# Kernel tuning notes

Measured on AMD Instinct MI355X. Metric: run time of the kernel, lower is better.

Reference implementation:

```python
import jax, jax.numpy as jnp
import numpy as np

B, L, H, P = 16, 4096, 512, 256
LN_EPS = 1e-6  # flax nnx.LayerNorm default


def setup_inputs() -> dict:
    key = jax.random.key(0)
    ks = jax.random.split(key, 9)
    dt_min, dt_max = 1e-3, 1e-1
    x = jax.random.normal(ks[0], (B, L, H), dtype=jnp.float32)
    # lecun-normal-like scaling for B (fan_in = H) and C (fan_in = P)
    return {
        "x": x,
        "log_lambda_re": jax.random.normal(ks[1], (P,), dtype=jnp.float32),
        "lambda_im": jax.random.normal(ks[2], (P,), dtype=jnp.float32) * 3.0,
        "B_re": jax.random.normal(ks[3], (P, H), dtype=jnp.float32) / np.sqrt(H),
        "B_im": jax.random.normal(ks[4], (P, H), dtype=jnp.float32) / np.sqrt(H),
        "C_re": jax.random.normal(ks[5], (H, P), dtype=jnp.float32) / np.sqrt(P),
        "C_im": jax.random.normal(ks[6], (H, P), dtype=jnp.float32) / np.sqrt(P),
        "D": jax.random.normal(ks[7], (H,), dtype=jnp.float32),
        "log_step": jax.random.uniform(ks[8], (P,), dtype=jnp.float32)
        * (np.log(dt_max) - np.log(dt_min)) + np.log(dt_min),
        "ln_scale": jnp.ones((H,), dtype=jnp.float32),
        "ln_bias": jnp.zeros((H,), dtype=jnp.float32),
    }


def _binary_operator(q_i, q_j):
    A_i, b_i = q_i
    A_j, b_j = q_j
    return (A_j * A_i, A_j * b_i + b_j)


def reference(x, log_lambda_re, lambda_im, B_re, B_im, C_re, C_im, D, log_step,
              ln_scale, ln_bias):
    Lambda = -jnp.exp(log_lambda_re) + 1j * lambda_im          # [P] complex
    B_tilde = B_re + 1j * B_im                                  # [P,H]
    C_tilde = C_re + 1j * C_im                                  # [H,P]
    step = jnp.exp(log_step)                                    # [P]
    # ZOH discretization
    Lambda_bar = jnp.exp(Lambda * step)                         # [P]
    B_bar = ((Lambda_bar - 1.0) / Lambda)[:, None] * B_tilde    # [P,H]
    # SSM via parallel associative scan over the length axis
    Bu = x @ B_bar.T                                            # [B,L,P] complex
    Lambda_el = jnp.broadcast_to(Lambda_bar, Bu.shape)          # [B,L,P]
    _, xs = jax.lax.associative_scan(_binary_operator, (Lambda_el, Bu), axis=-2)
    ys = 2.0 * (xs @ C_tilde.T).real                            # [B,L,H]
    y = ys + x * D
    y = jax.nn.gelu(y)
    # residual + LayerNorm
    z = x + y
    mean = jnp.mean(z, axis=-1, keepdims=True)
    var = jnp.var(z, axis=-1, keepdims=True)
    return (z - mean) * jax.lax.rsqrt(var + LN_EPS) * ln_scale + ln_bias
```

## Files before the change

### kernel.cpp

```cpp
#include <hip/hip_runtime.h>
#include <hip/hip_bf16.h>
#include <cstdint>
#include <cstddef>

typedef short bf16x8 __attribute__((ext_vector_type(8)));
typedef float f32x4  __attribute__((ext_vector_type(4)));

#define HH 512
#define PP 256
#define LL 4096
#define BBATCH 16
#define MM (BBATCH * LL)
#define NCHUNK 128
#define SCHUNK 32

__device__ __forceinline__ unsigned short f2bf(float f) {
  union { float f; unsigned u; } v; v.f = f;
  unsigned r = (v.u + 0x7FFFu + ((v.u >> 16) & 1u)) >> 16;
  return (unsigned short)r;
}
__device__ __forceinline__ float bf2f(unsigned short b) {
  return __uint_as_float(((unsigned)b) << 16);
}

__device__ __forceinline__ void async16(const void* g, void* l) {
  __builtin_amdgcn_global_load_lds(
      (const __attribute__((address_space(1))) unsigned*)g,
      (__attribute__((address_space(3))) unsigned*)l, 16, 0, 0);
}

__global__ void precompute_params(const float* __restrict__ llr_,
                                  const float* __restrict__ lim_,
                                  const float* __restrict__ lstep_,
                                  float* __restrict__ lam) {
  int p = threadIdx.x;
  if (p >= PP) return;
  float Lr = -expf(llr_[p]);
  float Li = lim_[p];
  float st = expf(lstep_[p]);
  float mag = expf(Lr * st);
  float ang = Li * st;
  float lbr = mag * cosf(ang);
  float lbi = mag * sinf(ang);
  float den = Lr * Lr + Li * Li;
  float nr = lbr - 1.f, ni = lbi;
  float cr = (nr * Lr + ni * Li) / den;
  float ci = (ni * Lr - nr * Li) / den;
  float m32 = expf(32.f * Lr * st);
  float a32r = m32 * cosf(32.f * ang);
  float a32i = m32 * sinf(32.f * ang);
  lam[p]            = lbr;
  lam[PP + p]       = lbi;
  lam[2 * PP + p]   = a32r;
  lam[3 * PP + p]   = a32i;
  lam[4 * PP + p]   = cr;
  lam[5 * PP + p]   = ci;
}

__global__ void build_weights(const float* __restrict__ B_re,
                              const float* __restrict__ B_im,
                              const float* __restrict__ C_re,
                              const float* __restrict__ C_im,
                              const float* __restrict__ lam,
                              unsigned short* __restrict__ Bcat,
                              unsigned short* __restrict__ Ccat) {
  int bid = blockIdx.x;
  int tid = threadIdx.x;
  if (bid < 512) {
    int n = bid;
    int p = (n < PP) ? n : n - PP;
    float cr = lam[4 * PP + p], ci = lam[5 * PP + p];
    for (int c = tid; c < HH; c += 256) {
      float br = B_re[(size_t)p * HH + c];
      float bi = B_im[(size_t)p * HH + c];
      float v = (n < PP) ? (cr * br - ci * bi) : (cr * bi + ci * br);
      Bcat[(size_t)n * HH + c] = f2bf(v);
    }
  } else {
    int h = bid - 512;
    for (int c = tid; c < HH; c += 256) {
      float v = (c < PP) ? 2.f * C_re[(size_t)h * PP + c]
                         : -2.f * C_im[(size_t)h * PP + (c - PP)];
      Ccat[(size_t)h * HH + c] = f2bf(v);
    }
  }
}

__global__ __launch_bounds__(256) void cvt_x_bf16(const float* __restrict__ x,
                                                  unsigned short* __restrict__ xb) {
  const float4* x4 = (const float4*)x;
  ushort4* o4 = (ushort4*)xb;
  int stride = 2048 * 256;
  for (int i = blockIdx.x * 256 + threadIdx.x; i < (MM * HH / 4); i += stride) {
    float4 v = x4[i];
    ushort4 o;
    o.x = f2bf(v.x); o.y = f2bf(v.y); o.z = f2bf(v.z); o.w = f2bf(v.w);
    o4[i] = o;
  }
}

template <int EPI>
__global__ __launch_bounds__(256) void gemm_bt(const unsigned short* __restrict__ A,
                                               const unsigned short* __restrict__ Bt,
                                               const unsigned short* xf,
                                               const float* __restrict__ Dv,
                                               unsigned short* Cout) {
  __shared__ __align__(16) unsigned short Asl[128 * 64];
  __shared__ __align__(16) unsigned short Bsl[128 * 64];
  const int tid = threadIdx.x, lane = tid & 63, w = tid >> 6;
  const int bid = blockIdx.x;
  const int logical = (bid & 7) * 256 + (bid >> 3);
  const int mt = logical >> 2, nt = logical & 3;
  const int m0 = mt * 128, n0 = nt * 128;
  const int r = lane & 15, g = lane >> 4;
  const int wm = (w >> 1) * 64, wn = (w & 1) * 64;

  const char* Ab = (const char*)A;
  const char* Bb = (const char*)Bt;
  char* AslB = (char*)Asl;
  char* BslB = (char*)Bsl;

  f32x4 acc[4][4];
#pragma unroll
  for (int a = 0; a < 4; ++a)
#pragma unroll
    for (int b = 0; b < 4; ++b) acc[a][b] = (f32x4){0.f, 0.f, 0.f, 0.f};

  const int swz = (r & 7) << 4;

  for (int kt = 0; kt < 512; kt += 64) {
#pragma unroll
    for (int j = 0; j < 4; ++j) {
      int idx = w * 4 + j;
      int W = idx * 1024 + lane * 16;
      int row = W >> 7;
      int colb = (W & 127) ^ ((row & 7) << 4);
      async16(Ab + (size_t)(m0 + row) * 1024 + kt * 2 + colb, AslB + W);
      async16(Bb + (size_t)(n0 + row) * 1024 + kt * 2 + colb, BslB + W);
    }
    asm volatile("s_waitcnt vmcnt(0)" ::: "memory");
    __syncthreads();
#pragma unroll
    for (int kk = 0; kk < 2; ++kk) {
      bf16x8 af[4], bv[4];
#pragma unroll
      for (int mi = 0; mi < 4; ++mi)
        af[mi] = *(const bf16x8*)(AslB + (wm + mi * 16 + r) * 128 +
                                  ((kk * 64 + g * 16) ^ swz));
#pragma unroll
      for (int ni = 0; ni < 4; ++ni)
        bv[ni] = *(const bf16x8*)(BslB + (wn + ni * 16 + r) * 128 +
                                  ((kk * 64 + g * 16) ^ swz));
#pragma unroll
      for (int mi = 0; mi < 4; ++mi)
#pragma unroll
        for (int ni = 0; ni < 4; ++ni)
          acc[mi][ni] = __builtin_amdgcn_mfma_f32_16x16x32_bf16(
              af[mi], bv[ni], acc[mi][ni], 0, 0, 0);
    }
    __syncthreads();
  }

#pragma unroll
  for (int mi = 0; mi < 4; ++mi) {
#pragma unroll
    for (int ni = 0; ni < 4; ++ni) {
      int col = n0 + wn + ni * 16 + r;
      float Dh = (EPI == 1) ? Dv[col] : 0.f;
#pragma unroll
      for (int j = 0; j < 4; ++j) {
        int row = m0 + wm + mi * 16 + g * 4 + j;
        float v = acc[mi][ni][j];
        if (EPI == 0) {
          Cout[(size_t)row * 512 + col] = f2bf(v);
        } else {
          float xv = bf2f(xf[(size_t)row * 512 + col]);
          float t = v + xv * Dh;
          float u = 0.7978845608028654f * (t + 0.044715f * t * t * t);
          float e = __expf(2.f * u);
          float th = 1.f - 2.f / (e + 1.f);
          float y = 0.5f * t * (1.f + th);
          Cout[(size_t)row * 512 + col] = f2bf(xv + y);
        }
      }
    }
  }
}

__global__ __launch_bounds__(256) void scan_carry(const unsigned short* __restrict__ Bu,
                                                  const float* __restrict__ lam,
                                                  float* __restrict__ carry) {
  int bid = blockIdx.x;
  int b = bid >> 7, c = bid & 127;
  int p = threadIdx.x;
  float ar = lam[p], ai = lam[PP + p];
  float sr = 0.f, si = 0.f;
  size_t base = ((size_t)b * LL + (size_t)c * SCHUNK) * 512;
#pragma unroll
  for (int i = 0; i < SCHUNK; ++i) {
    float ur = bf2f(Bu[base + (size_t)i * 512 + p]);
    float ui = bf2f(Bu[base + (size_t)i * 512 + 256 + p]);
    float nr = ar * sr - ai * si + ur;
    float ni = ar * si + ai * sr + ui;
    sr = nr; si = ni;
  }
  carry[(size_t)bid * 512 + p] = sr;
  carry[(size_t)bid * 512 + 256 + p] = si;
}

__global__ void scan_chain(float* __restrict__ carry, const float* __restrict__ lam) {
  int b = blockIdx.x;
  int p = threadIdx.x;
  float a32r = lam[2 * PP + p], a32i = lam[3 * PP + p];
  float sr = 0.f, si = 0.f;
  for (int c = 0; c < NCHUNK; ++c) {
    size_t idx = (size_t)(b * NCHUNK + c) * 512;
    float cr = carry[idx + p], ci = carry[idx + 256 + p];
    carry[idx + p] = sr;
    carry[idx + 256 + p] = si;
    float nr = cr + a32r * sr - a32i * si;
    float ni = ci + a32r * si + a32i * sr;
    sr = nr; si = ni;
  }
}

__global__ __launch_bounds__(256) void scan_final(const unsigned short* Bu,
                                                  const float* __restrict__ lam,
                                                  const float* __restrict__ carry,
                                                  unsigned short* xs) {
  int bid = blockIdx.x;
  int b = bid >> 7, c = bid & 127;
  int p = threadIdx.x;
  float ar = lam[p], ai = lam[PP + p];
  size_t cidx = (size_t)bid * 512;
  float sr = carry[cidx + p], si = carry[cidx + 256 + p];
  size_t base = ((size_t)b * LL + (size_t)c * SCHUNK) * 512;
#pragma unroll
  for (int i = 0; i < SCHUNK; ++i) {
    float ur = bf2f(Bu[base + (size_t)i * 512 + p]);
    float ui = bf2f(Bu[base + (size_t)i * 512 + 256 + p]);
    float nr = ar * sr - ai * si + ur;
    float ni = ar * si + ai * sr + ui;
    sr = nr; si = ni;
    xs[base + (size_t)i * 512 + p] = f2bf(sr);
    xs[base + (size_t)i * 512 + 256 + p] = f2bf(si);
  }
}

__global__ __launch_bounds__(256) void ln_kernel(const unsigned short* __restrict__ z,
                                                 const float* __restrict__ scale,
                                                 const float* __restrict__ bias,
                                                 float* __restrict__ out) {
  int tid = threadIdx.x, lane = tid & 63, wv = tid >> 6;
  int gw = blockIdx.x * 4 + wv;
  int c0 = lane * 8;
  float sc[8], bi[8];
#pragma unroll
  for (int j = 0; j < 8; ++j) { sc[j] = scale[c0 + j]; bi[j] = bias[c0 + j]; }
  for (int row = gw; row < MM; row += 8192) {
    uint4 zv = *(const uint4*)(z + (size_t)row * 512 + c0);
    float f[8];
    f[0] = __uint_as_float(zv.x << 16); f[1] = __uint_as_float(zv.x & 0xFFFF0000u);
    f[2] = __uint_as_float(zv.y << 16); f[3] = __uint_as_float(zv.y & 0xFFFF0000u);
    f[4] = __uint_as_float(zv.z << 16); f[5] = __uint_as_float(zv.z & 0xFFFF0000u);
    f[6] = __uint_as_float(zv.w << 16); f[7] = __uint_as_float(zv.w & 0xFFFF0000u);
    float s = 0.f, s2 = 0.f;
#pragma unroll
    for (int j = 0; j < 8; ++j) { s += f[j]; s2 += f[j] * f[j]; }
#pragma unroll
    for (int o = 32; o; o >>= 1) {
      s += __shfl_xor(s, o, 64);
      s2 += __shfl_xor(s2, o, 64);
    }
    float mean = s * (1.f / 512.f);
    float var = s2 * (1.f / 512.f) - mean * mean;
    float inv = rsqrtf(var + 1e-6f);
    float o8[8];
#pragma unroll
    for (int j = 0; j < 8; ++j) o8[j] = (f[j] - mean) * inv * sc[j] + bi[j];
    float4* op = (float4*)(out + (size_t)row * 512 + c0);
    op[0] = make_float4(o8[0], o8[1], o8[2], o8[3]);
    op[1] = make_float4(o8[4], o8[5], o8[6], o8[7]);
  }
}

extern "C" void kernel_launch(void* const* d_in, const int* in_sizes, int n_in,
                              void* d_out, int out_size, void* d_ws, size_t ws_size,
                              hipStream_t stream) {
  const float* x    = (const float*)d_in[0];
  const float* llr  = (const float*)d_in[1];
  const float* lim  = (const float*)d_in[2];
  const float* B_re = (const float*)d_in[3];
  const float* B_im = (const float*)d_in[4];
  const float* C_re = (const float*)d_in[5];
  const float* C_im = (const float*)d_in[6];
  const float* Dv   = (const float*)d_in[7];
  const float* lstep= (const float*)d_in[8];
  const float* lnsc = (const float*)d_in[9];
  const float* lnbi = (const float*)d_in[10];
  float* out = (float*)d_out;

  char* ws = (char*)d_ws;
  unsigned short* xb   = (unsigned short*)(ws);
  unsigned short* bu   = (unsigned short*)(ws + 67108864);
  unsigned short* bcat = (unsigned short*)(ws + 134217728);
  unsigned short* ccat = (unsigned short*)(ws + 134742016);
  float* lam           = (float*)(ws + 135266304);
  float* carry         = (float*)(ws + 135272448);

  precompute_params<<<1, 256, 0, stream>>>(llr, lim, lstep, lam);
  build_weights<<<1024, 256, 0, stream>>>(B_re, B_im, C_re, C_im, lam, bcat, ccat);
  cvt_x_bf16<<<2048, 256, 0, stream>>>(x, xb);
  gemm_bt<0><<<2048, 256, 0, stream>>>(xb, bcat, nullptr, nullptr, bu);
  scan_carry<<<2048, 256, 0, stream>>>(bu, lam, carry);
  scan_chain<<<16, 256, 0, stream>>>(carry, lam);
  scan_final<<<2048, 256, 0, stream>>>(bu, lam, carry, bu);
  gemm_bt<1><<<2048, 256, 0, stream>>>(bu, ccat, xb, Dv, xb);
  ln_kernel<<<2048, 256, 0, stream>>>(xb, lnsc, lnbi, out);
}
```

Baseline: 476.5 us.

## Double-buffer GEMM loads, interleave re/im in Bu, split carry chain hierarchically

The GEMM becomes persistent over four M tiles per block with double-buffered LDS. The next k-stage's async global-to-LDS loads are issued before the current stage's MFMAs, to overlap load latency with compute. Real and imaginary parts of Bu and xs are interleaved so each scan thread does one 32-bit load and store instead of two strided halves, and the weights are reordered to match. The serial 128-step carry chain on 16 blocks is replaced by a three-level scan (group reduce, 16-step chain using Lambda^256, group fixup) to add parallelism. The cost is fewer GEMM blocks (512), more LDS per block and two extra small launches.

```diff
diff --git a/kernel.cpp b/kernel.cpp
--- a/kernel.cpp
+++ b/kernel.cpp
@@ -13,6 +13,8 @@
 #define MM (BBATCH * LL)
 #define NCHUNK 128
 #define SCHUNK 32
+#define NGRP 16
+#define GCH 8
 
 __device__ __forceinline__ unsigned short f2bf(float f) {
   union { float f; unsigned u; } v; v.f = f;
@@ -49,12 +51,17 @@
   float m32 = expf(32.f * Lr * st);
   float a32r = m32 * cosf(32.f * ang);
   float a32i = m32 * sinf(32.f * ang);
+  float m256 = expf(256.f * Lr * st);
+  float a256r = m256 * cosf(256.f * ang);
+  float a256i = m256 * sinf(256.f * ang);
   lam[p]            = lbr;
   lam[PP + p]       = lbi;
   lam[2 * PP + p]   = a32r;
   lam[3 * PP + p]   = a32i;
   lam[4 * PP + p]   = cr;
   lam[5 * PP + p]   = ci;
+  lam[6 * PP + p]   = a256r;
+  lam[7 * PP + p]   = a256i;
 }
 
 __global__ void build_weights(const float* __restrict__ B_re,
@@ -68,19 +75,21 @@
   int tid = threadIdx.x;
   if (bid < 512) {
     int n = bid;
-    int p = (n < PP) ? n : n - PP;
+    int p = n >> 1;
+    int is_re = !(n & 1);
     float cr = lam[4 * PP + p], ci = lam[5 * PP + p];
     for (int c = tid; c < HH; c += 256) {
       float br = B_re[(size_t)p * HH + c];
       float bi = B_im[(size_t)p * HH + c];
-      float v = (n < PP) ? (cr * br - ci * bi) : (cr * bi + ci * br);
+      float v = is_re ? (cr * br - ci * bi) : (cr * bi + ci * br);
       Bcat[(size_t)n * HH + c] = f2bf(v);
     }
   } else {
     int h = bid - 512;
     for (int c = tid; c < HH; c += 256) {
-      float v = (c < PP) ? 2.f * C_re[(size_t)h * PP + c]
-                         : -2.f * C_im[(size_t)h * PP + (c - PP)];
+      int p = c >> 1;
+      float v = !(c & 1) ? 2.f * C_re[(size_t)h * PP + p]
+                         : -2.f * C_im[(size_t)h * PP + p];
       Ccat[(size_t)h * HH + c] = f2bf(v);
     }
   }
@@ -105,51 +114,67 @@
                                                const unsigned short* xf,
                                                const float* __restrict__ Dv,
                                                unsigned short* Cout) {
-  __shared__ __align__(16) unsigned short Asl[128 * 64];
-  __shared__ __align__(16) unsigned short Bsl[128 * 64];
+  __shared__ __align__(16) unsigned short As[2][8192];
+  __shared__ __align__(16) unsigned short Bs[2][8192];
   const int tid = threadIdx.x, lane = tid & 63, w = tid >> 6;
   const int bid = blockIdx.x;
-  const int logical = (bid & 7) * 256 + (bid >> 3);
-  const int mt = logical >> 2, nt = logical & 3;
-  const int m0 = mt * 128, n0 = nt * 128;
+  const int logical = (bid & 7) * 64 + (bid >> 3);
+  const int nt = logical & 3, mg = logical >> 2;
+  const int n0 = nt * 128;
   const int r = lane & 15, g = lane >> 4;
   const int wm = (w >> 1) * 64, wn = (w & 1) * 64;
-
+  const int swz = (r & 7) << 4;
+
+  int sW[4], srow[4], scol[4];
+#pragma unroll
+  for (int j = 0; j < 4; ++j) {
+    int idx = w * 4 + j;
+    int W = idx * 1024 + lane * 16;
+    sW[j] = W;
+    srow[j] = W >> 7;
+    scol[j] = (W & 127) ^ (((W >> 7) & 7) << 4);
+  }
   const char* Ab = (const char*)A;
   const char* Bb = (const char*)Bt;
-  char* AslB = (char*)Asl;
-  char* BslB = (char*)Bsl;
+  char* As0 = (char*)&As[0][0];
+  char* Bs0 = (char*)&Bs[0][0];
 
   f32x4 acc[4][4];
 #pragma unroll
-  for (int a = 0; a < 4; ++a)
-#pragma unroll
-    for (int b = 0; b < 4; ++b) acc[a][b] = (f32x4){0.f, 0.f, 0.f, 0.f};
-
-  const int swz = (r & 7) << 4;
-
-  for (int kt = 0; kt < 512; kt += 64) {
-#pragma unroll
-    for (int j = 0; j < 4; ++j) {
-      int idx = w * 4 + j;
-      int W = idx * 1024 + lane * 16;
-      int row = W >> 7;
-      int colb = (W & 127) ^ ((row & 7) << 4);
-      async16(Ab + (size_t)(m0 + row) * 1024 + kt * 2 + colb, AslB + W);
-      async16(Bb + (size_t)(n0 + row) * 1024 + kt * 2 + colb, BslB + W);
-    }
-    asm volatile("s_waitcnt vmcnt(0)" ::: "memory");
-    __syncthreads();
+  for (int a2 = 0; a2 < 4; ++a2)
+#pragma unroll
+    for (int b2 = 0; b2 < 4; ++b2) acc[a2][b2] = (f32x4){0.f, 0.f, 0.f, 0.f};
+
+#define STAGE_(buf_, s_) { \
+    int m0_ = (mg * 4 + ((s_) >> 3)) * 128; \
+    int kb_ = ((s_) & 7) * 128; \
+    char* dA_ = As0 + (buf_) * 16384; \
+    char* dB_ = Bs0 + (buf_) * 16384; \
+    _Pragma("unroll") \
+    for (int j = 0; j < 4; ++j) { \
+      async16(Ab + (size_t)(m0_ + srow[j]) * 1024 + kb_ + scol[j], dA_ + sW[j]); \
+      async16(Bb + (size_t)(n0  + srow[j]) * 1024 + kb_ + scol[j], dB_ + sW[j]); \
+    } }
+
+  STAGE_(0, 0);
+  asm volatile("s_waitcnt vmcnt(0)" ::: "memory");
+  __syncthreads();
+
+  int cur = 0;
+  for (int s = 0; s < 32; ++s) {
+    if (s < 31) STAGE_(cur ^ 1, s + 1);
+    const char* rdA = As0 + cur * 16384;
+    const char* rdB = Bs0 + cur * 16384;
 #pragma unroll
     for (int kk = 0; kk < 2; ++kk) {
       bf16x8 af[4], bv[4];
 #pragma unroll
       for (int mi = 0; mi < 4; ++mi)
-        af[mi] = *(const bf16x8*)(AslB + (wm + mi * 16 + r) * 128 +
+        af[mi] = *(const bf16x8*)(rdA + (wm + mi * 16 + r) * 128 +
                                   ((kk * 64 + g * 16) ^ swz));
 #pragma unroll
       for (int ni = 0; ni < 4; ++ni)
-        bv[ni] = *(const bf16x8*)(BslB + (wn + ni * 16 + r) * 128 +
+        bv[ni] = *(const bf16x8*)(rdB + (wn + ni * 16 + r) * 128 +
                                   ((kk * 64 + g * 16) ^ swz));
 #pragma unroll
       for (int mi = 0; mi < 4; ++mi)
@@ -158,33 +183,38 @@
           acc[mi][ni] = __builtin_amdgcn_mfma_f32_16x16x32_bf16(
               af[mi], bv[ni], acc[mi][ni], 0, 0, 0);
     }
+    if ((s & 7) == 7) {
+      int m0 = (mg * 4 + (s >> 3)) * 128;
+#pragma unroll
+      for (int mi = 0; mi < 4; ++mi)
+#pragma unroll
+        for (int ni = 0; ni < 4; ++ni) {
+          int col = n0 + wn + ni * 16 + r;
+          float Dh = (EPI == 1) ? Dv[col] : 0.f;
+#pragma unroll
+          for (int j = 0; j < 4; ++j) {
+            int row = m0 + wm + mi * 16 + g * 4 + j;
+            float v = acc[mi][ni][j];
+            if (EPI == 0) {
+              Cout[(size_t)row * 512 + col] = f2bf(v);
+            } else {
+              float xv = bf2f(xf[(size_t)row * 512 + col]);
+              float t = v + xv * Dh;
+              float u2 = 0.7978845608028654f * (t + 0.044715f * t * t * t);
+              float e = __expf(2.f * u2);
+              float th = 1.f - 2.f / (e + 1.f);
+              float y = 0.5f * t * (1.f + th);
+              Cout[(size_t)row * 512 + col] = f2bf(xv + y);
+            }
+            acc[mi][ni][j] = 0.f;
+          }
+        }
+    }
+    asm volatile("s_waitcnt vmcnt(0)" ::: "memory");
     __syncthreads();
-  }
-
-#pragma unroll
-  for (int mi = 0; mi < 4; ++mi) {
-#pragma unroll
-    for (int ni = 0; ni < 4; ++ni) {
-      int col = n0 + wn + ni * 16 + r;
-      float Dh = (EPI == 1) ? Dv[col] : 0.f;
-#pragma unroll
-      for (int j = 0; j < 4; ++j) {
-        int row = m0 + wm + mi * 16 + g * 4 + j;
-        float v = acc[mi][ni][j];
-        if (EPI == 0) {
-          Cout[(size_t)row * 512 + col] = f2bf(v);
-        } else {
-          float xv = bf2f(xf[(size_t)row * 512 + col]);
-          float t = v + xv * Dh;
-          float u = 0.7978845608028654f * (t + 0.044715f * t * t * t);
-          float e = __expf(2.f * u);
-          float th = 1.f - 2.f / (e + 1.f);
-          float y = 0.5f * t * (1.f + th);
-          Cout[(size_t)row * 512 + col] = f2bf(xv + y);
-        }
-      }
-    }
-  }
+    cur ^= 1;
+  }
+#undef STAGE_
 }
 
 __global__ __launch_bounds__(256) void scan_carry(const unsigned short* __restrict__ Bu,
@@ -198,52 +228,93 @@
   size_t base = ((size_t)b * LL + (size_t)c * SCHUNK) * 512;
 #pragma unroll
   for (int i = 0; i < SCHUNK; ++i) {
-    float ur = bf2f(Bu[base + (size_t)i * 512 + p]);
-    float ui = bf2f(Bu[base + (size_t)i * 512 + 256 + p]);
+    unsigned u = ((const unsigned*)(Bu + base + (size_t)i * 512))[p];
+    float ur = bf2f((unsigned short)(u & 0xFFFFu));
+    float ui = bf2f((unsigned short)(u >> 16));
     float nr = ar * sr - ai * si + ur;
     float ni = ar * si + ai * sr + ui;
     sr = nr; si = ni;
   }
-  carry[(size_t)bid * 512 + p] = sr;
-  carry[(size_t)bid * 512 + 256 + p] = si;
-}
-
-__global__ void scan_chain(float* __restrict__ carry, const float* __restrict__ lam) {
+  ((float2*)(carry + (size_t)bid * 512))[p] = make_float2(sr, si);
+}
+
+__global__ void chain_a(const float* __restrict__ carry,
+                        const float* __restrict__ lam,
+                        float* __restrict__ gcarry) {
+  int bid = blockIdx.x;
+  int b = bid >> 4, g2 = bid & 15;
+  int p = threadIdx.x;
+  float ar = lam[2 * PP + p], ai = lam[3 * PP + p];
+  float sr = 0.f, si = 0.f;
+#pragma unroll
+  for (int i = 0; i < GCH; ++i) {
+    int c = g2 * GCH + i;
+    float2 cv = ((const float2*)(carry + (size_t)(b * NCHUNK + c) * 512))[p];
+    float nr = cv.x + ar * sr - ai * si;
+    float ni = cv.y + ar * si + ai * sr;
+    sr = nr; si = ni;
+  }
+  ((float2*)(gcarry + (size_t)bid * 512))[p] = make_float2(sr, si);
+}
+
+__global__ void chain_b(const float* __restrict__ gcarry,
+                        const float* __restrict__ lam,
+                        float* __restrict__ gstate) {
   int b = blockIdx.x;
   int p = threadIdx.x;
-  float a32r = lam[2 * PP + p], a32i = lam[3 * PP + p];
+  float ar = lam[6 * PP + p], ai = lam[7 * PP + p];
   float sr = 0.f, si = 0.f;
-  for (int c = 0; c < NCHUNK; ++c) {
-    size_t idx = (size_t)(b * NCHUNK + c) * 512;
-    float cr = carry[idx + p], ci = carry[idx + 256 + p];
-    carry[idx + p] = sr;
-    carry[idx + 256 + p] = si;
-    float nr = cr + a32r * sr - a32i * si;
-    float ni = ci + a32r * si + a32i * sr;
-    sr = nr; si = ni;
-  }
-}
-
-__global__ __launch_bounds__(256) void scan_final(const unsigned short* Bu,
+#pragma unroll
+  for (int g2 = 0; g2 < NGRP; ++g2) {
+    float2 cv = ((const float2*)(gcarry + (size_t)(b * NGRP + g2) * 512))[p];
+    ((float2*)(gstate + (size_t)(b * NGRP + g2) * 512))[p] = make_float2(sr, si);
+    float nr = cv.x + ar * sr - ai * si;
+    float ni = cv.y + ar * si + ai * sr;
+    sr = nr; si = ni;
+  }
+}
+
+__global__ void chain_c(float* carry,
+                        const float* __restrict__ lam,
+                        const float* __restrict__ gstate) {
+  int bid = blockIdx.x;
+  int b = bid >> 4, g2 = bid & 15;
+  int p = threadIdx.x;
+  float ar = lam[2 * PP + p], ai = lam[3 * PP + p];
+  float2 s0 = ((const float2*)(gstate + (size_t)bid * 512))[p];
+  float sr = s0.x, si = s0.y;
+#pragma unroll
+  for (int i = 0; i < GCH; ++i) {
+    int c = g2 * GCH + i;
+    float2* slot = ((float2*)(carry + (size_t)(b * NCHUNK + c) * 512)) + p;
+    float2 cv = *slot;
+    *slot = make_float2(sr, si);
+    float nr = cv.x + ar * sr - ai * si;
+    float ni = cv.y + ar * si + ai * sr;
+    sr = nr; si = ni;
+  }
+}
+
+__global__ __launch_bounds__(256) void scan_final(unsigned short* Bu,
                                                   const float* __restrict__ lam,
-                                                  const float* __restrict__ carry,
-                                                  unsigned short* xs) {
+                                                  const float* __restrict__ carry) {
   int bid = blockIdx.x;
   int b = bid >> 7, c = bid & 127;
   int p = threadIdx.x;
   float ar = lam[p], ai = lam[PP + p];
-  size_t cidx = (size_t)bid * 512;
-  float sr = carry[cidx + p], si = carry[cidx + 256 + p];
+  float2 s0 = ((const float2*)(carry + (size_t)bid * 512))[p];
+  float sr = s0.x, si = s0.y;
   size_t base = ((size_t)b * LL + (size_t)c * SCHUNK) * 512;
 #pragma unroll
   for (int i = 0; i < SCHUNK; ++i) {
-    float ur = bf2f(Bu[base + (size_t)i * 512 + p]);
-    float ui = bf2f(Bu[base + (size_t)i * 512 + 256 + p]);
+    unsigned* slot = ((unsigned*)(Bu + base + (size_t)i * 512)) + p;
+    unsigned u = *slot;
+    float ur = bf2f((unsigned short)(u & 0xFFFFu));
+    float ui = bf2f((unsigned short)(u >> 16));
     float nr = ar * sr - ai * si + ur;
     float ni = ar * si + ai * sr + ui;
     sr = nr; si = ni;
-    xs[base + (size_t)i * 512 + p] = f2bf(sr);
-    xs[base + (size_t)i * 512 + 256 + p] = f2bf(si);
+    *slot = (unsigned)f2bf(sr) | ((unsigned)f2bf(si) << 16);
   }
 }
 
@@ -306,15 +377,19 @@
   unsigned short* bcat = (unsigned short*)(ws + 134217728);
   unsigned short* ccat = (unsigned short*)(ws + 134742016);
   float* lam           = (float*)(ws + 135266304);
-  float* carry         = (float*)(ws + 135272448);
+  float* carry         = (float*)(ws + 135274496);
+  float* gcarry        = (float*)(ws + 139468800);
+  float* gstate        = (float*)(ws + 139993088);
 
   precompute_params<<<1, 256, 0, stream>>>(llr, lim, lstep, lam);
   build_weights<<<1024, 256, 0, stream>>>(B_re, B_im, C_re, C_im, lam, bcat, ccat);
   cvt_x_bf16<<<2048, 256, 0, stream>>>(x, xb);
-  gemm_bt<0><<<2048, 256, 0, stream>>>(xb, bcat, nullptr, nullptr, bu);
+  gemm_bt<0><<<512, 256, 0, stream>>>(xb, bcat, nullptr, nullptr, bu);
   scan_carry<<<2048, 256, 0, stream>>>(bu, lam, carry);
-  scan_chain<<<16, 256, 0, stream>>>(carry, lam);
-  scan_final<<<2048, 256, 0, stream>>>(bu, lam, carry, bu);
-  gemm_bt<1><<<2048, 256, 0, stream>>>(bu, ccat, xb, Dv, xb);
+  chain_a<<<256, 256, 0, stream>>>(carry, lam, gcarry);
+  chain_b<<<16, 256, 0, stream>>>(gcarry, lam, gstate);
+  chain_c<<<256, 256, 0, stream>>>(carry, lam, gstate);
+  scan_final<<<2048, 256, 0, stream>>>(bu, lam, carry);
+  gemm_bt<1><<<512, 256, 0, stream>>>(bu, ccat, xb, Dv, xb);
   ln_kernel<<<2048, 256, 0, stream>>>(xb, lnsc, lnbi, out);
 }
```

Result: no change. 472.8 us (-0.8%).
